# Kernel tuning notes

Hardware: AMD Instinct MI355X
Metric: run time of the kernel (lower is better)

Reference implementation:

```python
import jax, jax.numpy as jnp
import numpy as np

PAD = 200000   # padding index = all_features_num
D = 128        # input_dim (embedding dim)
H = 256        # hidden_dim
K = 15         # item_num (top-k)
M = 4          # multi_head


def _cos(a, b, eps=1e-8):
    # torch.cosine_similarity semantics with eps clamp on norms
    na = jnp.maximum(jnp.linalg.norm(a, axis=-1), eps)
    nb = jnp.maximum(jnp.linalg.norm(b, axis=-1), eps)
    return jnp.sum(a * b, axis=-1) / (na * nb)


def _rnn_input(x, emb):
    # x: [..., T, F] int. Fields :-2 are embedded+summed, field -2 is time.
    t = x[..., -2].astype(jnp.float32)
    dt = jnp.concatenate([jnp.zeros_like(t[..., :1]), jnp.diff(t, axis=-1)], axis=-1)
    e = emb[x[..., :-2]].sum(axis=-2)          # [..., T, D]
    x_self = e[:, 0:1, -1:, :]                  # [B,1,1,D] (self item placed at last slot of session 0)
    return jnp.concatenate([e, dt[..., None]], axis=-1), x_self


def _time_rnn(seq, W, U, b, wt, return_all=False):
    # Time-aware GRU. seq: [N, T, in+1]; last channel is delta-time feeding a decay gate.
    f, dt = seq[..., :-1], seq[..., -1:]
    N = seq.shape[0]
    g_in = jnp.einsum('nti,ij->ntj', f, W) + b   # precompute input projections [N,T,3H]

    def step(h, inp):
        g, d = inp                               # g:[N,3H], d:[N,1]
        decay = jnp.exp(-jax.nn.relu(d * wt))    # time-aware decay of hidden state
        hd = h * decay
        u = hd @ U
        z = jax.nn.sigmoid(g[:, :H] + u[:, :H])
        r = jax.nn.sigmoid(g[:, H:2 * H] + u[:, H:2 * H])
        n = jnp.tanh(g[:, 2 * H:] + r * u[:, 2 * H:])
        h_new = (1.0 - z) * hd + z * n
        return h_new, h_new

    h0 = jnp.zeros((N, H), seq.dtype)
    h_last, hs = jax.lax.scan(step, h0, (jnp.swapaxes(g_in, 0, 1), jnp.swapaxes(dt, 0, 1)))
    return jnp.swapaxes(hs, 0, 1) if return_all else h_last


def setup_inputs() -> dict:
    key = jax.random.key(0)
    ks = jax.random.split(key, 20)
    def n(k, shape, s=0.05):
        return jax.random.normal(k, shape, jnp.float32) * s
    x = jax.random.randint(ks[0], (512, 16, 64, 8), 0, PAD, dtype=jnp.int32)
    x_continuous = jax.random.randint(ks[1], (128, 128, 8), 0, PAD, dtype=jnp.int32)
    self_loc = jax.random.randint(ks[2], (512,), 0, 64, dtype=jnp.int32)
    emb = n(ks[3], (PAD + 1, D)).at[PAD].set(0.0)  # padding_idx row = 0
    return {
        'x': x, 'x_continuous': x_continuous, 'self_loc': self_loc, 'emb': emb,
        'W_rnn': n(ks[4], (2 * D, 3 * H)), 'U_rnn': n(ks[5], (H, 3 * H)), 'b_rnn': n(ks[6], (3 * H,)),
        'wt_rnn': jax.random.uniform(ks[7], (H,), jnp.float32, 0.0, 1e-5),
        'W_c': n(ks[8], (D, 3 * H)), 'U_c': n(ks[9], (H, 3 * H)), 'b_c': n(ks[10], (3 * H,)),
        'wt_c': jax.random.uniform(ks[11], (H,), jnp.float32, 0.0, 1e-5),
        'Wv': n(ks[12], (2 * H, M)), 'bv': n(ks[13], (M,)),
        'W0': n(ks[14], (D + (2 + M) * H, 1024)), 'b0': n(ks[15], (1024,)),
        'W1': n(ks[16], (1024, 512)), 'b1': n(ks[17], (512,)),
        'W2': n(ks[18], (512, 256)), 'b2': n(ks[19], (256,)),
        'Wp': n(jax.random.fold_in(key, 99), (256, 1)), 'bp': jnp.zeros((1,), jnp.float32),
    }


def reference(x, x_continuous, self_loc, emb, W_rnn, U_rnn, b_rnn, wt_rnn,
              W_c, U_c, b_c, wt_c, Wv, bv, W0, b0, W1, b1, W2, b2, Wp, bp):
    B = x.shape[0]
    label_len = B // x_continuous.shape[0]
    # ---- get_top_k: cosine sim + topk + gather ----
    real = x[..., 0] != PAD                         # [B,S,L]
    bidx = jnp.arange(B)
    e_self = emb[x[bidx, 0, self_loc, -3]]           # [B,D]
    e_items = emb[x[..., -3]]                        # [B,S,L,D]
    cos = _cos(e_self[:, None, None, :], e_items)    # [B,S,L]
    neg = jnp.min(jnp.where(real, cos, jnp.inf)) - 1.0
    sim = jnp.where(real, cos, neg)
    top_idx = jnp.sort(jax.lax.top_k(sim, K)[1], axis=-1)      # [B,S,K]
    x_top = jnp.take_along_axis(x, top_idx[..., None], axis=2)  # [B,S,K,F]
    x_top = x_top.at[:, 0, -1].set(x[bidx, 0, self_loc])
    # ---- rnn inputs ----
    xs, x_self = _rnn_input(x_top, emb)              # [B,S,K,D+1], [B,1,1,D]
    xs = jnp.concatenate([jnp.broadcast_to(x_self, xs.shape[:-1] + (D,)), xs], axis=-1)
    xs = xs.reshape(-1, K, 2 * D + 1)                # [B*S,K,2D+1]
    xc, _ = _rnn_input(x_continuous[:, None], emb)
    xc = xc[:, 0]                                    # [B',L2,D+1]
    # ---- RNNs ----
    h = _time_rnn(xs, W_rnn, U_rnn, b_rnn, wt_rnn).reshape(B, -1, H)   # [B,S,H]
    h_cont = _time_rnn(xc, W_c, U_c, b_c, wt_c, return_all=True)[:, -label_len:, :].reshape(B, H)
    # ---- multi-head attention over sessions ----
    a1 = jnp.concatenate([h, jnp.broadcast_to(h[:, :1], h.shape)], axis=-1) @ Wv + bv  # [B,S,M]
    a2 = jax.nn.softmax(jnp.tanh(a1), axis=1)
    h_att = jnp.einsum('bsm,bsh->bmh', a2, h).reshape(B, M * H)
    hh = jnp.concatenate([x_self.reshape(B, D), h[:, 0], h_att, h_cont], axis=-1)
    # ---- predict MLP (dropout = identity in eval) ----
    lr = lambda v: jnp.where(v > 0, v, 0.01 * v)     # LeakyReLU(0.01)
    z = lr(hh @ W0 + b0)
    z = lr(z @ W1 + b1)
    z = lr(z @ W2 + b2)
    return jax.nn.sigmoid(z @ Wp + bp)               # [B,1]
```

## Files before the change

### kernel.cpp

```cpp
#include <hip/hip_runtime.h>
#include <hip/hip_bf16.h>


#define PAD_TOK 200000
#define DD 128
#define HH 256
#define KK 15
#define BB 512
#define SS 16
#define II 64

typedef __bf16 bf16x8 __attribute__((ext_vector_type(8)));
typedef __bf16 bf16x4 __attribute__((ext_vector_type(4)));
typedef float f32x4 __attribute__((ext_vector_type(4)));
#define MFMA16 __builtin_amdgcn_mfma_f32_16x16x32_bf16
#define MFMA8 __builtin_amdgcn_mfma_f32_16x16x32_fp8_fp8

__device__ __forceinline__ float sigm(float x) { return 1.f / (1.f + __expf(-x)); }
__device__ __forceinline__ float tanh_fast(float x) {
  x = fminf(fmaxf(x, -15.f), 15.f);
  float e2 = __expf(2.f * x);
  return (e2 - 1.f) / (e2 + 1.f);
}
__device__ __forceinline__ float bfu(unsigned u16) { return __uint_as_float(u16 << 16); }

__device__ __forceinline__ unsigned char f2fp8(float x) {
  unsigned u = __float_as_uint(x);
  unsigned s = (u >> 31) << 7;
  int e = (int)((u >> 23) & 0xff) - 127;
  if (e < -6) return (unsigned char)s;
  unsigned m = (u >> 20) & 7;
  unsigned rest = u & 0xFFFFF;
  if (rest > 0x80000 || (rest == 0x80000 && (m & 1))) {
    ++m;
    if (m == 8) {
      m = 0;
      ++e;
    }
  }
  if (e > 7) {
    e = 7;
    m = 6;
  }
  return (unsigned char)(s | ((unsigned)(e + 7) << 3) | m);
}

__device__ __forceinline__ unsigned cvt2fp8(float a, float b) {
#if __has_builtin(__builtin_amdgcn_cvt_pk_fp8_f32)
  return (unsigned)__builtin_amdgcn_cvt_pk_fp8_f32(a, b, 0, false) & 0xffffu;
#else
  return (unsigned)f2fp8(a) | ((unsigned)f2fp8(b) << 8);
#endif
}

__global__ __launch_bounds__(128) void k_build_cont(const int* __restrict__ xc,
                                                    const float* __restrict__ emb,
                                                    __hip_bfloat16* __restrict__ ec,
                                                    float* __restrict__ dtc) {
  int p = blockIdx.x, t = blockIdx.y, d = threadIdx.x;
  const int* xr = xc + ((size_t)p * 128 + t) * 8;
  float acc = 0.f;
#pragma unroll
  for (int jj = 0; jj < 6; ++jj) acc += emb[(size_t)xr[jj] * DD + d];
  ec[((size_t)p * 128 + t) * DD + d] = __float2bfloat16(acc);
  if (d == 0) dtc[p * 128 + t] = (t > 0) ? ((float)xr[6] - (float)xr[-2]) : 0.f;
}

__global__ __launch_bounds__(64) void k_pack(const float* __restrict__ B,
                                             __bf16* __restrict__ out) {
  int kt = blockIdx.x, tile = blockIdx.y, lane = threadIdx.x;
  const float* src = B + (size_t)(kt * 32 + (lane >> 4) * 8) * 768 + tile * 16 + (lane & 15);
  __bf16* o = out + (((size_t)(kt * 48 + tile) * 64 + lane) * 8);
#pragma unroll
  for (int i = 0; i < 8; ++i) o[i] = (__bf16)src[(size_t)i * 768];
}

__global__ __launch_bounds__(64) void k_pack8(const float* __restrict__ B,
                                              unsigned char* __restrict__ out) {
  int kt = blockIdx.x, tile = blockIdx.y, lane = threadIdx.x;
  const float* src = B + (size_t)(kt * 32 + (lane >> 4) * 8) * 768 + tile * 16 + (lane & 15);
  unsigned char* o = out + (((size_t)(kt * 48 + tile) * 64 + lane) * 8);
#pragma unroll
  for (int i = 0; i < 8; ++i) o[i] = f2fp8(src[(size_t)i * 768] * 8.f);
}

__global__ __launch_bounds__(64) void k_packN(const float* __restrict__ B,
                                              __bf16* __restrict__ out, int N) {
  int kt = blockIdx.x, tile = blockIdx.y, lane = threadIdx.x;
  const float* src = B + (size_t)(kt * 32 + (lane >> 4) * 8) * N + tile * 16 + (lane & 15);
  __bf16* o = out + (((size_t)kt * gridDim.y + tile) * 64 + lane) * 8;
#pragma unroll
  for (int i = 0; i < 8; ++i) o[i] = (__bf16)src[(size_t)i * N];
}

__global__ __launch_bounds__(512) void k_gemm_g(const __hip_bfloat16* __restrict__ A,
                                                const __bf16* __restrict__ pB,
                                                const float* __restrict__ bias,
                                                __bf16* __restrict__ G2) {
  const int wv = threadIdx.x >> 6, lane = threadIdx.x & 63;
  const int lr = lane & 15, lg = lane >> 4;
  const int r0 = blockIdx.x * 32;
  f32x4 z4 = {0.f, 0.f, 0.f, 0.f};
  f32x4 acc[2][6];
#pragma unroll
  for (int mt = 0; mt < 2; ++mt)
#pragma unroll
    for (int n = 0; n < 6; ++n) acc[mt][n] = z4;
#pragma unroll
  for (int kt = 0; kt < 4; ++kt) {
    bf16x8 a[2];
#pragma unroll
    for (int mt = 0; mt < 2; ++mt)
      a[mt] = *(const bf16x8*)(A + (size_t)(r0 + mt * 16 + lr) * 128 + kt * 32 + lg * 8);
#pragma unroll
    for (int n = 0; n < 6; ++n) {
      bf16x8 b = *(const bf16x8*)(pB + (((size_t)kt * 48 + wv * 6 + n) * 64 + lane) * 8);
      acc[0][n] = MFMA16(a[0], b, acc[0][n], 0, 0, 0);
      acc[1][n] = MFMA16(a[1], b, acc[1][n], 0, 0, 0);
    }
  }
#pragma unroll
  for (int mt = 0; mt < 2; ++mt)
#pragma unroll
    for (int n = 0; n < 6; ++n) {
      int col = wv * 96 + n * 16 + lr;
      int gate = col >> 8, wvc = (col >> 5) & 7, nt = (col >> 4) & 1;
      float bc = bias[col];
#pragma unroll
      for (int r = 0; r < 4; ++r) {
        int row = r0 + mt * 16 + lg * 4 + r;
        G2[(size_t)row * 1024 + wvc * 128 + lr * 8 + gate * 2 + nt] = (__bf16)(acc[mt][n][r] + bc);
      }
    }
}

__device__ void cont_body(char* smem, const __bf16* __restrict__ G2,
                          const float* __restrict__ dtc,
                          const unsigned char* __restrict__ pU8,
                          const float* __restrict__ wt, float* __restrict__ hcont,
                          int blk) {
  unsigned char(*hbuf)[16 * 256] = (unsigned char(*)[16 * 256])smem;
  unsigned char(*uL)[30 * 512] = (unsigned char(*)[30 * 512])(smem + 8192);
  float* dl = (float*)(smem + 8192 + 122880);
  const int wv = threadIdx.x >> 6, lane = threadIdx.x & 63;
  const int lr = lane & 15, lg = lane >> 4;
  const int p0 = blk * 16;
  for (int idx = threadIdx.x; idx < 2048; idx += 512)
    dl[idx] = dtc[(p0 + (idx >> 7)) * 128 + (idx & 127)];
  for (int i = threadIdx.x; i < 8 * 30 * 64; i += 512) {
    int l = i & 63;
    int fw = i >> 6;
    int f = fw % 30;
    int w = fw / 30;
    int kt = 3 + f / 6;
    int gi = f % 6;
    *(uint2*)&uL[w][(size_t)f * 512 + l * 8] =
        *(const uint2*)(pU8 + (((size_t)kt * 48 + (gi >> 1) * 16 + w * 2 + (gi & 1)) * 64 + l) * 8);
  }
  long fr[3][6];
#pragma unroll
  for (int kt = 0; kt < 3; ++kt)
#pragma unroll
    for (int gi = 0; gi < 6; ++gi)
      fr[kt][gi] =
          *(const long*)(pU8 + (((size_t)kt * 48 + (gi >> 1) * 16 + wv * 2 + (gi & 1)) * 64 + lane) * 8);

  float wtv[2];
#pragma unroll
  for (int nt = 0; nt < 2; ++nt) wtv[nt] = wt[wv * 32 + nt * 16 + lr];
  float h[2][4];
#pragma unroll
  for (int nt = 0; nt < 2; ++nt)
#pragma unroll
    for (int r = 0; r < 4; ++r) h[nt][r] = 0.f;

  const uint4* G2v = (const uint4*)G2;
  const size_t gb0 = (size_t)(p0 + lg * 4) * 16384 + wv * 16 + lr;
  uint4 Gv[4], Gn[4];
#pragma unroll
  for (int r = 0; r < 4; ++r) Gv[r] = G2v[gb0 + (size_t)r * 16384];
  __syncthreads();

  for (int t = 0; t < 128; ++t) {
    unsigned char* hb = hbuf[t & 1];
    float hd[2][4];
#pragma unroll
    for (int r = 0; r < 4; ++r) {
      float dtv = dl[(lg * 4 + r) * 128 + t];
#pragma unroll
      for (int nt = 0; nt < 2; ++nt) hd[nt][r] = h[nt][r] * __expf(-fmaxf(dtv * wtv[nt], 0.f));
    }
    const int c0 = wv * 32 + lr, c1 = wv * 32 + 16 + lr;
#pragma unroll
    for (int r = 0; r < 4; ++r) {
      int row = lg * 4 + r;
      int sw = (row & 15) << 3;
      unsigned pk = cvt2fp8(hd[0][r] * 16.f, hd[1][r] * 16.f);
      hb[row * 256 + (c0 ^ sw)] = (unsigned char)pk;
      hb[row * 256 + (c1 ^ sw)] = (unsigned char)(pk >> 8);
    }
    if (t < 127) {
#pragma unroll
      for (int r = 0; r < 4; ++r) Gn[r] = G2v[gb0 + (size_t)r * 16384 + (size_t)(t + 1) * 128];
    }
    __syncthreads();
    f32x4 acc[3][2];
#pragma unroll
    for (int g = 0; g < 3; ++g)
#pragma unroll
      for (int nt = 0; nt < 2; ++nt) acc[g][nt] = f32x4{0.f, 0.f, 0.f, 0.f};
#pragma unroll
    for (int kt = 0; kt < 8; ++kt) {
      long a = *(const long*)&hb[lr * 256 + ((kt * 32 + lg * 8) ^ ((lr & 15) << 3))];
#pragma unroll
      for (int gi = 0; gi < 6; ++gi) {
        long b = (kt < 3) ? fr[kt][gi]
                          : *(const long*)&uL[wv][(size_t)((kt - 3) * 6 + gi) * 512 + lane * 8];
        acc[gi >> 1][gi & 1] = MFMA8(a, b, acc[gi >> 1][gi & 1], 0, 0, 0);
      }
    }
#pragma unroll
    for (int nt = 0; nt < 2; ++nt)
#pragma unroll
      for (int r = 0; r < 4; ++r) {
        unsigned uz = nt ? (Gv[r].x >> 16) : (Gv[r].x & 0xffffu);
        unsigned ur = nt ? (Gv[r].y >> 16) : (Gv[r].y & 0xffffu);
        unsigned un = nt ? (Gv[r].z >> 16) : (Gv[r].z & 0xffffu);
        const float us = 0.0078125f;
        float zz = sigm(bfu(uz) + acc[0][nt][r] * us);
        float rr = sigm(bfu(ur) + acc[1][nt][r] * us);
        float nn = tanh_fast(bfu(un) + rr * acc[2][nt][r] * us);
        float hnew = (1.f - zz) * hd[nt][r] + zz * nn;
        h[nt][r] = hnew;
        if (t >= 124)
          hcont[((size_t)(p0 + lg * 4 + r) * 4 + (t - 124)) * 256 + wv * 32 + nt * 16 + lr] = hnew;
      }
#pragma unroll
    for (int r = 0; r < 4; ++r) Gv[r] = Gn[r];
  }
}

__device__ void main_body(char* smem, const int* __restrict__ x,
                          const int* __restrict__ self_loc,
                          const float* __restrict__ emb,
                          const __bf16* __restrict__ pWs, const __bf16* __restrict__ pWe,
                          const __bf16* __restrict__ pU, const float* __restrict__ bg,
                          const float* __restrict__ wt, __bf16* __restrict__ em,
                          float* __restrict__ xself, float* __restrict__ hmain,
                          int blk) {
  __bf16(*hbuf)[32 * 256] = (__bf16(*)[32 * 256])smem;
  float* dl = (float*)(smem + 32768);
  float* esL = (float*)(smem + 34944);
  float* nsL = (float*)(smem + 35968);
  __bf16* xsbf = (__bf16*)(smem + 36000);
  float* simL = (float*)(smem + 36544);
  int* tpxL = (int*)(smem + 44736);
  const int tid = threadIdx.x;
  const int wv = tid >> 6, lane = tid & 63;
  const int lr = lane & 15, lg = lane >> 4;
  const int n0 = blk * 32;
  const int b0 = n0 >> 4;
  f32x4 z4 = {0.f, 0.f, 0.f, 0.f};

  if (tid < 256) {
    int bb = tid >> 7, d = tid & 127;
    int bgl = b0 + bb;
    int tok = x[((size_t)(bgl * SS) * II + self_loc[bgl]) * 8 + 5];
    esL[bb * 128 + d] = emb[(size_t)tok * DD + d];
  }
  __syncthreads();
  if (tid < 128) {
    int bb = tid >> 6, l = tid & 63;
    float v0 = esL[bb * 128 + l], v1 = esL[bb * 128 + 64 + l];
    float ss = v0 * v0 + v1 * v1;
    for (int o = 32; o; o >>= 1) ss += __shfl_xor(ss, o);
    if (l == 0) nsL[bb] = fmaxf(sqrtf(ss), 1e-8f);
  }
  __syncthreads();
  for (int it = 0; it < 16; ++it) {
    int pr = it * 128 + (tid >> 2);
    int row = pr >> 6, item = pr & 63, q = tid & 3;
    const int* xr = x + ((size_t)(n0 + row) * II + item) * 8;
    int tok = xr[5];
    int first = xr[0];
    const float4* ep = (const float4*)(emb + (size_t)tok * DD + q * 32);
    const float4* sp = (const float4*)(esL + (row >> 4) * 128 + q * 32);
    float dot = 0.f, ss = 0.f;
#pragma unroll
    for (int j = 0; j < 8; ++j) {
      float4 a = ep[j];
      float4 e = sp[j];
      dot += a.x * e.x + a.y * e.y + a.z * e.z + a.w * e.w;
      ss += a.x * a.x + a.y * a.y + a.z * a.z + a.w * a.w;
    }
    dot += __shfl_xor(dot, 1);
    ss += __shfl_xor(ss, 1);
    dot += __shfl_xor(dot, 2);
    ss += __shfl_xor(ss, 2);
    if (q == 0)
      simL[row * 64 + item] =
          (first != PAD_TOK) ? dot / (fmaxf(sqrtf(ss), 1e-8f) * nsL[row >> 4]) : -3.0f;
  }
  __syncthreads();
  for (int it = 0; it < 4; ++it) {
    int pr = it * 512 + tid;
    int row = pr >> 6, item = pr & 63;
    float s = simL[row * 64 + item];
    int rank = 0;
    for (int j = 0; j < 64; ++j) {
      float o = simL[row * 64 + j];
      rank += (o > s) || (o == s && j < item);
    }
    bool sel = rank < KK;
    unsigned long long mask = __ballot(sel);
    if (sel) {
      int pos = __popcll(mask & ((1ull << item) - 1ull));
      tpxL[row * KK + pos] = item;
    }
  }
  __syncthreads();
  for (int t = 0; t < KK; ++t) {
    int rr = tid >> 5, q = tid & 31;
#pragma unroll
    for (int pass = 0; pass < 2; ++pass) {
      int rloc = pass * 16 + rr;
      int ng = n0 + rloc;
      int bb = ng >> 4, s = ng & 15;
      bool ovr = (s == 0) && (t == KK - 1);
      int item = ovr ? self_loc[bb] : tpxL[rloc * KK + t];
      const int* xr = x + ((size_t)ng * II + item) * 8;
      float4 a4 = {0.f, 0.f, 0.f, 0.f};
#pragma unroll
      for (int jj = 0; jj < 6; ++jj) {
        float4 v = *(const float4*)(emb + (size_t)xr[jj] * DD + q * 4);
        a4.x += v.x;
        a4.y += v.y;
        a4.z += v.z;
        a4.w += v.w;
      }
      bf16x4 ov = {(__bf16)a4.x, (__bf16)a4.y, (__bf16)a4.z, (__bf16)a4.w};
      *(bf16x4*)(em + ((size_t)t * 8192 + ng) * DD + q * 4) = ov;
      if (ovr) {
        *(float4*)(xself + bb * DD + q * 4) = a4;
        *(bf16x4*)(xsbf + (bb - b0) * 128 + q * 4) = ov;
      }
      if (q == 0) {
        float dtv = 0.f;
        if (t > 0) {
          int pitem = tpxL[rloc * KK + t - 1];
          dtv = (float)xr[6] - (float)x[((size_t)ng * II + pitem) * 8 + 6];
        }
        dl[t * 32 + rloc] = dtv;
      }
    }
  }
  __syncthreads();

  float wtv[2], bz[2], br[2], bn[2];
#pragma unroll
  for (int nt = 0; nt < 2; ++nt) {
    int c = wv * 32 + nt * 16 + lr;
    wtv[nt] = wt[c];
    bz[nt] = bg[c];
    br[nt] = bg[c + 256];
    bn[nt] = bg[c + 512];
  }
  float h[2][2][4];
#pragma unroll
  for (int mt = 0; mt < 2; ++mt)
#pragma unroll
    for (int nt = 0; nt < 2; ++nt)
#pragma unroll
      for (int r = 0; r < 4; ++r) h[mt][nt][r] = 0.f;

  for (int t = 0; t < KK; ++t) {
    __bf16* hb = hbuf[t & 1];
#pragma unroll
    for (int mt = 0; mt < 2; ++mt)
#pragma unroll
      for (int r = 0; r < 4; ++r) {
        float dtv = dl[t * 32 + mt * 16 + lg * 4 + r];
        int row = mt * 16 + lg * 4 + r;
#pragma unroll
        for (int nt = 0; nt < 2; ++nt) {
          float hdv = h[mt][nt][r] * __expf(-fmaxf(dtv * wtv[nt], 0.f));
          hb[((row * 256) + (wv * 32 + nt * 16 + lr)) ^ ((row & 7) << 3)] = (__bf16)hdv;
        }
      }
    __syncthreads();
#pragma unroll
    for (int ntp = 0; ntp < 2; ++ntp) {
      f32x4 acc[4][2];
#pragma unroll
      for (int a4 = 0; a4 < 4; ++a4)
#pragma unroll
        for (int mt = 0; mt < 2; ++mt) acc[a4][mt] = z4;
#pragma unroll 2
      for (int kt = 0; kt < 8; ++kt) {
        bf16x8 a[2];
#pragma unroll
        for (int mt = 0; mt < 2; ++mt) {
          int row = mt * 16 + lr;
          int s = ((row * 256) + (kt * 32 + lg * 8)) ^ ((row & 7) << 3);
          a[mt] = *(const bf16x8*)&hb[s];
        }
#pragma unroll
        for (int g = 0; g < 3; ++g) {
          const int ai = (g < 2) ? g : 3;
          bf16x8 b = *(const bf16x8*)(pU + (((size_t)kt * 48 + g * 16 + wv * 2 + ntp) * 64 + lane) * 8);
#pragma unroll
          for (int mt = 0; mt < 2; ++mt) acc[ai][mt] = MFMA16(a[mt], b, acc[ai][mt], 0, 0, 0);
        }
      }
#pragma unroll 2
      for (int kt = 0; kt < 8; ++kt) {
        bf16x8 a[2];
#pragma unroll
        for (int mt = 0; mt < 2; ++mt) {
          if (kt < 4)
            a[mt] = *(const bf16x8*)(xsbf + mt * 128 + kt * 32 + lg * 8);
          else
            a[mt] = *(const bf16x8*)(em + ((size_t)t * 8192 + n0 + mt * 16 + lr) * 128 +
                                     (kt - 4) * 32 + lg * 8);
        }
        const __bf16* pB = (kt < 4) ? (pWs + (size_t)kt * 48 * 512)
                                    : (pWe + (size_t)(kt - 4) * 48 * 512);
#pragma unroll
        for (int g = 0; g < 3; ++g) {
          bf16x8 b = *(const bf16x8*)(pB + (((size_t)g * 16 + wv * 2 + ntp) * 64 + lane) * 8);
#pragma unroll
          for (int mt = 0; mt < 2; ++mt) acc[g][mt] = MFMA16(a[mt], b, acc[g][mt], 0, 0, 0);
        }
      }
#pragma unroll
      for (int mt = 0; mt < 2; ++mt)
#pragma unroll
        for (int r = 0; r < 4; ++r) {
          float dtv = dl[t * 32 + mt * 16 + lg * 4 + r];
          float hdv = h[mt][ntp][r] * __expf(-fmaxf(dtv * wtv[ntp], 0.f));
          float zz = sigm(acc[0][mt][r] + bz[ntp]);
          float rr = sigm(acc[1][mt][r] + br[ntp]);
          float nn = tanh_fast(acc[2][mt][r] + bn[ntp] + rr * acc[3][mt][r]);
          h[mt][ntp][r] = (1.f - zz) * hdv + zz * nn;
        }
    }
  }
  __syncthreads();
#pragma unroll
  for (int mt = 0; mt < 2; ++mt)
#pragma unroll
    for (int nt = 0; nt < 2; ++nt)
#pragma unroll
      for (int r = 0; r < 4; ++r)
        hmain[(size_t)(n0 + mt * 16 + lg * 4 + r) * 256 + wv * 32 + nt * 16 + lr] = h[mt][nt][r];
}

__global__ __launch_bounds__(512) void k_rnn_fused(
    const __bf16* __restrict__ G2, const float* __restrict__ dtc,
    const unsigned char* __restrict__ pU8, const float* __restrict__ wt_c,
    float* __restrict__ hcont, const int* __restrict__ x,
    const int* __restrict__ self_loc, const float* __restrict__ emb,
    const __bf16* __restrict__ pWs, const __bf16* __restrict__ pWe,
    const __bf16* __restrict__ pU, const float* __restrict__ b_rnn,
    const float* __restrict__ wt_m, __bf16* __restrict__ em,
    float* __restrict__ xself, float* __restrict__ hmain) {
  __shared__ __align__(16) char smem[8192 + 122880 + 8192];
  if (blockIdx.x < 8)
    cont_body(smem, G2, dtc, pU8, wt_c, hcont, blockIdx.x);
  else
    main_body(smem, x, self_loc, emb, pWs, pWe, pU, b_rnn, wt_m, em, xself, hmain,
              blockIdx.x - 8);
}

__global__ __launch_bounds__(256) void k_att(const float* __restrict__ hmain,
                                             const float* __restrict__ xself,
                                             const float* __restrict__ hc,
                                             const float* __restrict__ Wv,
                                             const float* __restrict__ bv,
                                             float* __restrict__ hh,
                                             __bf16* __restrict__ hh_bf) {
  int b = blockIdx.x, tid = threadIdx.x;
  __shared__ float hl[16 * 256];
  __shared__ float aa[16 * 4];
  for (int idx = tid; idx < 4096; idx += 256) hl[idx] = hmain[(size_t)b * SS * HH + idx];
  __syncthreads();
  if (tid < 64) {
    int s = tid >> 2, m = tid & 3;
    float acc = bv[m];
    for (int j = 0; j < 256; ++j)
      acc += hl[s * 256 + j] * Wv[j * 4 + m] + hl[j] * Wv[(256 + j) * 4 + m];
    aa[s * 4 + m] = tanh_fast(acc);
  }
  __syncthreads();
  if (tid < 4) {
    int m = tid;
    float mx = -1e30f;
    for (int s = 0; s < 16; ++s) mx = fmaxf(mx, aa[s * 4 + m]);
    float sum = 0.f;
    for (int s = 0; s < 16; ++s) sum += __expf(aa[s * 4 + m] - mx);
    float inv = 1.f / sum;
    for (int s = 0; s < 16; ++s) aa[s * 4 + m] = __expf(aa[s * 4 + m] - mx) * inv;
  }
  __syncthreads();
  float a0 = 0.f, a1 = 0.f, a2 = 0.f, a3 = 0.f;
  for (int s = 0; s < 16; ++s) {
    float hv = hl[s * 256 + tid];
    a0 = fmaf(aa[s * 4 + 0], hv, a0);
    a1 = fmaf(aa[s * 4 + 1], hv, a1);
    a2 = fmaf(aa[s * 4 + 2], hv, a2);
    a3 = fmaf(aa[s * 4 + 3], hv, a3);
  }
  float* hb = hh + (size_t)b * 1664;
  __bf16* hf = hh_bf + (size_t)b * 1664;
  hb[384 + 0 * 256 + tid] = a0;
  hb[384 + 1 * 256 + tid] = a1;
  hb[384 + 2 * 256 + tid] = a2;
  hb[384 + 3 * 256 + tid] = a3;
  hf[384 + 0 * 256 + tid] = (__bf16)a0;
  hf[384 + 1 * 256 + tid] = (__bf16)a1;
  hf[384 + 2 * 256 + tid] = (__bf16)a2;
  hf[384 + 3 * 256 + tid] = (__bf16)a3;
  if (tid < 128) {
    hb[tid] = xself[b * DD + tid];
    hf[tid] = (__bf16)xself[b * DD + tid];
  }
  hb[128 + tid] = hl[tid];
  hf[128 + tid] = (__bf16)hl[tid];
  float hcv = hc[(size_t)b * HH + tid];
  hb[1408 + tid] = hcv;
  hf[1408 + tid] = (__bf16)hcv;
}

__global__ __launch_bounds__(512) void k_mlp_mfma(const __bf16* __restrict__ A,
                                                  const __bf16* __restrict__ pW,
                                                  const float* __restrict__ bias,
                                                  __bf16* __restrict__ C, int K, int N) {
  const int wv = threadIdx.x >> 6, lane = threadIdx.x & 63;
  const int lr = lane & 15, lg = lane >> 4;
  const int r0 = blockIdx.y * 32;
  const int c0 = blockIdx.x * 256;
  const int NT = N >> 4;
  const int KT = K >> 5;
  f32x4 acc[2][2];
#pragma unroll
  for (int mt = 0; mt < 2; ++mt)
#pragma unroll
    for (int nt = 0; nt < 2; ++nt) acc[mt][nt] = f32x4{0.f, 0.f, 0.f, 0.f};
  for (int kt = 0; kt < KT; ++kt) {
    bf16x8 a[2];
#pragma unroll
    for (int mt = 0; mt < 2; ++mt)
      a[mt] = *(const bf16x8*)(A + (size_t)(r0 + mt * 16 + lr) * K + kt * 32 + lg * 8);
#pragma unroll
    for (int nt = 0; nt < 2; ++nt) {
      bf16x8 b = *(const bf16x8*)(pW + (((size_t)kt * NT + (c0 >> 4) + wv * 2 + nt) * 64 + lane) * 8);
#pragma unroll
      for (int mt = 0; mt < 2; ++mt) acc[mt][nt] = MFMA16(a[mt], b, acc[mt][nt], 0, 0, 0);
    }
  }
#pragma unroll
  for (int nt = 0; nt < 2; ++nt) {
    int col = c0 + wv * 32 + nt * 16 + lr;
    float bc = bias[col];
#pragma unroll
    for (int mt = 0; mt < 2; ++mt)
#pragma unroll
      for (int r = 0; r < 4; ++r) {
        float v = acc[mt][nt][r] + bc;
        v = v > 0.f ? v : 0.01f * v;
        C[(size_t)(r0 + mt * 16 + lg * 4 + r) * N + col] = (__bf16)v;
      }
  }
}

__global__ __launch_bounds__(64) void k_head(const __bf16* __restrict__ A,
                                             const float* __restrict__ Wp,
                                             const float* __restrict__ bp,
                                             float* __restrict__ out) {
  int row = blockIdx.x, l = threadIdx.x;
  float acc = 0.f;
  for (int j = l; j < 256; j += 64) acc = fmaf((float)A[(size_t)row * 256 + j], Wp[j], acc);
  for (int o = 32; o; o >>= 1) acc += __shfl_xor(acc, o);
  if (l == 0) out[row] = 1.f / (1.f + __expf(-(acc + bp[0])));
}

extern "C" void kernel_launch(void* const* d_in, const int* in_sizes, int n_in,
                              void* d_out, int out_size, void* d_ws, size_t ws_size,
                              hipStream_t stream) {
  const int* x = (const int*)d_in[0];
  const int* xc = (const int*)d_in[1];
  const int* self_loc = (const int*)d_in[2];
  const float* emb = (const float*)d_in[3];
  const float* W_rnn = (const float*)d_in[4];
  const float* U_rnn = (const float*)d_in[5];
  const float* b_rnn = (const float*)d_in[6];
  const float* wt_rnn = (const float*)d_in[7];
  const float* W_c = (const float*)d_in[8];
  const float* U_c = (const float*)d_in[9];
  const float* b_c = (const float*)d_in[10];
  const float* wt_c = (const float*)d_in[11];
  const float* Wv = (const float*)d_in[12];
  const float* bv = (const float*)d_in[13];
  const float* W0 = (const float*)d_in[14];
  const float* b0 = (const float*)d_in[15];
  const float* W1 = (const float*)d_in[16];
  const float* b1 = (const float*)d_in[17];
  const float* W2 = (const float*)d_in[18];
  const float* b2 = (const float*)d_in[19];
  const float* Wp = (const float*)d_in[20];
  const float* bp = (const float*)d_in[21];
  float* out = (float*)d_out;

  char* ws = (char*)d_ws;
  size_t cur = 0;
  auto alloc = [&](size_t bytes) {
    char* p = ws + cur;
    cur += (bytes + 255) & ~(size_t)255;
    return p;
  };
  float* xself = (float*)alloc((size_t)BB * DD * 4);
  float* dtc = (float*)alloc((size_t)128 * 128 * 4);
  float* hcont = (float*)alloc((size_t)BB * HH * 4);
  float* hh = (float*)alloc((size_t)BB * 1664 * 4);
  __bf16* hh_bf = (__bf16*)alloc((size_t)BB * 1664 * 2);
  __bf16* z0 = (__bf16*)alloc((size_t)BB * 1024 * 2);
  __bf16* z1 = (__bf16*)alloc((size_t)BB * 512 * 2);
  __bf16* z2 = (__bf16*)alloc((size_t)BB * 256 * 2);
  float* hmain = (float*)alloc((size_t)8192 * HH * 4);
  __hip_bfloat16* ec = (__hip_bfloat16*)alloc((size_t)16384 * DD * 2);
  __bf16* em = (__bf16*)alloc((size_t)KK * 8192 * DD * 2);
  __bf16* G2 = (__bf16*)alloc((size_t)16384 * 1024 * 2);
  __bf16* pWs = (__bf16*)alloc((size_t)4 * 48 * 64 * 8 * 2);
  __bf16* pWe = (__bf16*)alloc((size_t)4 * 48 * 64 * 8 * 2);
  __bf16* pU = (__bf16*)alloc((size_t)8 * 48 * 64 * 8 * 2);
  __bf16* pWc = (__bf16*)alloc((size_t)4 * 48 * 64 * 8 * 2);
  unsigned char* pU8 = (unsigned char*)alloc((size_t)8 * 48 * 64 * 8);
  __bf16* pW0 = (__bf16*)alloc((size_t)52 * 64 * 64 * 8 * 2);
  __bf16* pW1 = (__bf16*)alloc((size_t)32 * 32 * 64 * 8 * 2);
  __bf16* pW2 = (__bf16*)alloc((size_t)16 * 16 * 64 * 8 * 2);
  (void)ws_size;

  hipLaunchKernelGGL(k_build_cont, dim3(128, 128), dim3(128), 0, stream, xc, emb, ec, dtc);
  hipLaunchKernelGGL(k_pack, dim3(4, 48), dim3(64), 0, stream, W_c, pWc);
  hipLaunchKernelGGL(k_pack8, dim3(8, 48), dim3(64), 0, stream, U_c, pU8);
  hipLaunchKernelGGL(k_gemm_g, dim3(512), dim3(512), 0, stream, ec, pWc, b_c, G2);
  hipLaunchKernelGGL(k_pack, dim3(4, 48), dim3(64), 0, stream, W_rnn, pWs);
  hipLaunchKernelGGL(k_pack, dim3(4, 48), dim3(64), 0, stream, W_rnn + 128 * 768, pWe);
  hipLaunchKernelGGL(k_pack, dim3(8, 48), dim3(64), 0, stream, U_rnn, pU);
  hipLaunchKernelGGL(k_packN, dim3(52, 64), dim3(64), 0, stream, W0, pW0, 1024);
  hipLaunchKernelGGL(k_packN, dim3(32, 32), dim3(64), 0, stream, W1, pW1, 512);
  hipLaunchKernelGGL(k_packN, dim3(16, 16), dim3(64), 0, stream, W2, pW2, 256);
  hipLaunchKernelGGL(k_rnn_fused, dim3(264), dim3(512), 0, stream, G2, dtc, pU8, wt_c,
                     hcont, x, self_loc, emb, pWs, pWe, pU, b_rnn, wt_rnn, em, xself,
                     hmain);
  hipLaunchKernelGGL(k_att, dim3(BB), dim3(256), 0, stream, hmain, xself, hcont, Wv, bv, hh,
                     hh_bf);
  hipLaunchKernelGGL(k_mlp_mfma, dim3(4, 16), dim3(512), 0, stream, hh_bf, pW0, b0, z0,
                     1664, 1024);
  hipLaunchKernelGGL(k_mlp_mfma, dim3(2, 16), dim3(512), 0, stream, z0, pW1, b1, z1, 1024,
                     512);
  hipLaunchKernelGGL(k_mlp_mfma, dim3(1, 16), dim3(512), 0, stream, z1, pW2, b2, z2, 512,
                     256);
  hipLaunchKernelGGL(k_head, dim3(BB), dim3(64), 0, stream, z2, Wp, bp, out);
}
```

Baseline: 764.1 us.

## Halve rows per main-RNN block to double grid parallelism

Each main-body block now processes 16 session rows (one batch element) instead of 32, and the grid grows from 264 to 520 blocks. Shared-memory offsets, the similarity/top-k loops, the gather loop and the GRU MFMA tiles are all reduced to a single M-tile. The aim is to fill more CUs during the latency-bound 15-step recurrence. In exchange, every U/W weight fragment is loaded from global memory twice as often per row, and each block has less MFMA work to hide latency with.

```diff
diff --git a/kernel.cpp b/kernel.cpp
--- a/kernel.cpp
+++ b/kernel.cpp
@@ -248,43 +248,40 @@
                           const float* __restrict__ wt, __bf16* __restrict__ em,
                           float* __restrict__ xself, float* __restrict__ hmain,
                           int blk) {
-  __bf16(*hbuf)[32 * 256] = (__bf16(*)[32 * 256])smem;
-  float* dl = (float*)(smem + 32768);
-  float* esL = (float*)(smem + 34944);
-  float* nsL = (float*)(smem + 35968);
-  __bf16* xsbf = (__bf16*)(smem + 36000);
-  float* simL = (float*)(smem + 36544);
-  int* tpxL = (int*)(smem + 44736);
+  __bf16(*hbuf)[16 * 256] = (__bf16(*)[16 * 256])smem;
+  float* dl = (float*)(smem + 16384);
+  float* esL = (float*)(smem + 17408);
+  float* nsL = (float*)(smem + 17920);
+  __bf16* xsbf = (__bf16*)(smem + 17952);
+  float* simL = (float*)(smem + 18240);
+  int* tpxL = (int*)(smem + 22336);
   const int tid = threadIdx.x;
   const int wv = tid >> 6, lane = tid & 63;
   const int lr = lane & 15, lg = lane >> 4;
-  const int n0 = blk * 32;
+  const int n0 = blk * 16;
   const int b0 = n0 >> 4;
   f32x4 z4 = {0.f, 0.f, 0.f, 0.f};
 
-  if (tid < 256) {
-    int bb = tid >> 7, d = tid & 127;
-    int bgl = b0 + bb;
-    int tok = x[((size_t)(bgl * SS) * II + self_loc[bgl]) * 8 + 5];
-    esL[bb * 128 + d] = emb[(size_t)tok * DD + d];
-  }
-  __syncthreads();
   if (tid < 128) {
-    int bb = tid >> 6, l = tid & 63;
-    float v0 = esL[bb * 128 + l], v1 = esL[bb * 128 + 64 + l];
+    int tok = x[((size_t)(b0 * SS) * II + self_loc[b0]) * 8 + 5];
+    esL[tid] = emb[(size_t)tok * DD + tid];
+  }
+  __syncthreads();
+  if (tid < 64) {
+    float v0 = esL[tid], v1 = esL[64 + tid];
     float ss = v0 * v0 + v1 * v1;
     for (int o = 32; o; o >>= 1) ss += __shfl_xor(ss, o);
-    if (l == 0) nsL[bb] = fmaxf(sqrtf(ss), 1e-8f);
-  }
-  __syncthreads();
-  for (int it = 0; it < 16; ++it) {
+    if (tid == 0) nsL[0] = fmaxf(sqrtf(ss), 1e-8f);
+  }
+  __syncthreads();
+  for (int it = 0; it < 8; ++it) {
     int pr = it * 128 + (tid >> 2);
     int row = pr >> 6, item = pr & 63, q = tid & 3;
     const int* xr = x + ((size_t)(n0 + row) * II + item) * 8;
     int tok = xr[5];
     int first = xr[0];
     const float4* ep = (const float4*)(emb + (size_t)tok * DD + q * 32);
-    const float4* sp = (const float4*)(esL + (row >> 4) * 128 + q * 32);
+    const float4* sp = (const float4*)(esL + q * 32);
     float dot = 0.f, ss = 0.f;
 #pragma unroll
     for (int j = 0; j < 8; ++j) {
@@ -299,10 +296,10 @@
     ss += __shfl_xor(ss, 2);
     if (q == 0)
       simL[row * 64 + item] =
-          (first != PAD_TOK) ? dot / (fmaxf(sqrtf(ss), 1e-8f) * nsL[row >> 4]) : -3.0f;
-  }
-  __syncthreads();
-  for (int it = 0; it < 4; ++it) {
+          (first != PAD_TOK) ? dot / (fmaxf(sqrtf(ss), 1e-8f) * nsL[0]) : -3.0f;
+  }
+  __syncthreads();
+  for (int it = 0; it < 2; ++it) {
     int pr = it * 512 + tid;
     int row = pr >> 6, item = pr & 63;
     float s = simL[row * 64 + item];
@@ -319,15 +316,12 @@
     }
   }
   __syncthreads();
-  for (int t = 0; t < KK; ++t) {
-    int rr = tid >> 5, q = tid & 31;
-#pragma unroll
-    for (int pass = 0; pass < 2; ++pass) {
-      int rloc = pass * 16 + rr;
+  {
+    int rloc = tid >> 5, q = tid & 31;
+    for (int t = 0; t < KK; ++t) {
       int ng = n0 + rloc;
-      int bb = ng >> 4, s = ng & 15;
-      bool ovr = (s == 0) && (t == KK - 1);
-      int item = ovr ? self_loc[bb] : tpxL[rloc * KK + t];
+      bool ovr = (rloc == 0) && (t == KK - 1);
+      int item = ovr ? self_loc[b0] : tpxL[rloc * KK + t];
       const int* xr = x + ((size_t)ng * II + item) * 8;
       float4 a4 = {0.f, 0.f, 0.f, 0.f};
 #pragma unroll
@@ -341,8 +335,8 @@
       bf16x4 ov = {(__bf16)a4.x, (__bf16)a4.y, (__bf16)a4.z, (__bf16)a4.w};
       *(bf16x4*)(em + ((size_t)t * 8192 + ng) * DD + q * 4) = ov;
       if (ovr) {
-        *(float4*)(xself + bb * DD + q * 4) = a4;
-        *(bf16x4*)(xsbf + (bb - b0) * 128 + q * 4) = ov;
+        *(float4*)(xself + b0 * DD + q * 4) = a4;
+        *(bf16x4*)(xsbf + q * 4) = ov;
       }
       if (q == 0) {
         float dtv = 0.f;
@@ -350,7 +344,7 @@
           int pitem = tpxL[rloc * KK + t - 1];
           dtv = (float)xr[6] - (float)x[((size_t)ng * II + pitem) * 8 + 6];
         }
-        dl[t * 32 + rloc] = dtv;
+        dl[t * 16 + rloc] = dtv;
       }
     }
   }
@@ -365,94 +359,74 @@
     br[nt] = bg[c + 256];
     bn[nt] = bg[c + 512];
   }
-  float h[2][2][4];
-#pragma unroll
-  for (int mt = 0; mt < 2; ++mt)
-#pragma unroll
-    for (int nt = 0; nt < 2; ++nt)
-#pragma unroll
-      for (int r = 0; r < 4; ++r) h[mt][nt][r] = 0.f;
+  float h[2][4];
+#pragma unroll
+  for (int nt = 0; nt < 2; ++nt)
+#pragma unroll
+    for (int r = 0; r < 4; ++r) h[nt][r] = 0.f;
 
   for (int t = 0; t < KK; ++t) {
     __bf16* hb = hbuf[t & 1];
 #pragma unroll
-    for (int mt = 0; mt < 2; ++mt)
-#pragma unroll
-      for (int r = 0; r < 4; ++r) {
-        float dtv = dl[t * 32 + mt * 16 + lg * 4 + r];
-        int row = mt * 16 + lg * 4 + r;
-#pragma unroll
-        for (int nt = 0; nt < 2; ++nt) {
-          float hdv = h[mt][nt][r] * __expf(-fmaxf(dtv * wtv[nt], 0.f));
-          hb[((row * 256) + (wv * 32 + nt * 16 + lr)) ^ ((row & 7) << 3)] = (__bf16)hdv;
-        }
-      }
+    for (int r = 0; r < 4; ++r) {
+      float dtv = dl[t * 16 + lg * 4 + r];
+      int row = lg * 4 + r;
+#pragma unroll
+      for (int nt = 0; nt < 2; ++nt) {
+        float hdv = h[nt][r] * __expf(-fmaxf(dtv * wtv[nt], 0.f));
+        hb[((row * 256) + (wv * 32 + nt * 16 + lr)) ^ ((row & 7) << 3)] = (__bf16)hdv;
+      }
+    }
     __syncthreads();
 #pragma unroll
     for (int ntp = 0; ntp < 2; ++ntp) {
-      f32x4 acc[4][2];
-#pragma unroll
-      for (int a4 = 0; a4 < 4; ++a4)
-#pragma unroll
-        for (int mt = 0; mt < 2; ++mt) acc[a4][mt] = z4;
+      f32x4 acc[4];
+#pragma unroll
+      for (int a4 = 0; a4 < 4; ++a4) acc[a4] = z4;
 #pragma unroll 2
       for (int kt = 0; kt < 8; ++kt) {
-        bf16x8 a[2];
-#pragma unroll
-        for (int mt = 0; mt < 2; ++mt) {
-          int row = mt * 16 + lr;
-          int s = ((row * 256) + (kt * 32 + lg * 8)) ^ ((row & 7) << 3);
-          a[mt] = *(const bf16x8*)&hb[s];
-        }
+        int row = lr;
+        int s = ((row * 256) + (kt * 32 + lg * 8)) ^ ((row & 7) << 3);
+        bf16x8 a = *(const bf16x8*)&hb[s];
 #pragma unroll
         for (int g = 0; g < 3; ++g) {
           const int ai = (g < 2) ? g : 3;
           bf16x8 b = *(const bf16x8*)(pU + (((size_t)kt * 48 + g * 16 + wv * 2 + ntp) * 64 + lane) * 8);
-#pragma unroll
-          for (int mt = 0; mt < 2; ++mt) acc[ai][mt] = MFMA16(a[mt], b, acc[ai][mt], 0, 0, 0);
+          acc[ai] = MFMA16(a, b, acc[ai], 0, 0, 0);
         }
       }
 #pragma unroll 2
       for (int kt = 0; kt < 8; ++kt) {
-        bf16x8 a[2];
-#pragma unroll
-        for (int mt = 0; mt < 2; ++mt) {
-          if (kt < 4)
-            a[mt] = *(const bf16x8*)(xsbf + mt * 128 + kt * 32 + lg * 8);
-          else
-            a[mt] = *(const bf16x8*)(em + ((size_t)t * 8192 + n0 + mt * 16 + lr) * 128 +
-                                     (kt - 4) * 32 + lg * 8);
-        }
+        bf16x8 a;
+        if (kt < 4)
+          a = *(const bf16x8*)(xsbf + kt * 32 + lg * 8);
+        else
+          a = *(const bf16x8*)(em + ((size_t)t * 8192 + n0 + lr) * 128 + (kt - 4) * 32 + lg * 8);
         const __bf16* pB = (kt < 4) ? (pWs + (size_t)kt * 48 * 512)
                                     : (pWe + (size_t)(kt - 4) * 48 * 512);
 #pragma unroll
         for (int g = 0; g < 3; ++g) {
           bf16x8 b = *(const bf16x8*)(pB + (((size_t)g * 16 + wv * 2 + ntp) * 64 + lane) * 8);
-#pragma unroll
-          for (int mt = 0; mt < 2; ++mt) acc[g][mt] = MFMA16(a[mt], b, acc[g][mt], 0, 0, 0);
+          acc[g] = MFMA16(a, b, acc[g], 0, 0, 0);
         }
       }
 #pragma unroll
-      for (int mt = 0; mt < 2; ++mt)
-#pragma unroll
-        for (int r = 0; r < 4; ++r) {
-          float dtv = dl[t * 32 + mt * 16 + lg * 4 + r];
-          float hdv = h[mt][ntp][r] * __expf(-fmaxf(dtv * wtv[ntp], 0.f));
-          float zz = sigm(acc[0][mt][r] + bz[ntp]);
-          float rr = sigm(acc[1][mt][r] + br[ntp]);
-          float nn = tanh_fast(acc[2][mt][r] + bn[ntp] + rr * acc[3][mt][r]);
-          h[mt][ntp][r] = (1.f - zz) * hdv + zz * nn;
-        }
-    }
-  }
-  __syncthreads();
-#pragma unroll
-  for (int mt = 0; mt < 2; ++mt)
-#pragma unroll
-    for (int nt = 0; nt < 2; ++nt)
-#pragma unroll
-      for (int r = 0; r < 4; ++r)
-        hmain[(size_t)(n0 + mt * 16 + lg * 4 + r) * 256 + wv * 32 + nt * 16 + lr] = h[mt][nt][r];
+      for (int r = 0; r < 4; ++r) {
+        float dtv = dl[t * 16 + lg * 4 + r];
+        float hdv = h[ntp][r] * __expf(-fmaxf(dtv * wtv[ntp], 0.f));
+        float zz = sigm(acc[0][r] + bz[ntp]);
+        float rr = sigm(acc[1][r] + br[ntp]);
+        float nn = tanh_fast(acc[2][r] + bn[ntp] + rr * acc[3][r]);
+        h[ntp][r] = (1.f - zz) * hdv + zz * nn;
+      }
+    }
+  }
+  __syncthreads();
+#pragma unroll
+  for (int nt = 0; nt < 2; ++nt)
+#pragma unroll
+    for (int r = 0; r < 4; ++r)
+      hmain[(size_t)(n0 + lg * 4 + r) * 256 + wv * 32 + nt * 16 + lr] = h[nt][r];
 }
 
 __global__ __launch_bounds__(512) void k_rnn_fused(
@@ -650,7 +624,7 @@
   hipLaunchKernelGGL(k_packN, dim3(52, 64), dim3(64), 0, stream, W0, pW0, 1024);
   hipLaunchKernelGGL(k_packN, dim3(32, 32), dim3(64), 0, stream, W1, pW1, 512);
   hipLaunchKernelGGL(k_packN, dim3(16, 16), dim3(64), 0, stream, W2, pW2, 256);
-  hipLaunchKernelGGL(k_rnn_fused, dim3(264), dim3(512), 0, stream, G2, dtc, pU8, wt_c,
+  hipLaunchKernelGGL(k_rnn_fused, dim3(520), dim3(512), 0, stream, G2, dtc, pU8, wt_c,
                      hcont, x, self_loc, emb, pWs, pWe, pU, b_rnn, wt_rnn, em, xself,
                      hmain);
   hipLaunchKernelGGL(k_att, dim3(BB), dim3(256), 0, stream, hmain, xself, hcont, Wv, bv, hh,
```

After: 791.2 us. +3.6%, slower.
